# Performance work log

Measured on AMD Instinct MI355X. Metric: run time of the kernel, lower is better.

## Reference

```python
import jax, jax.numpy as jnp
import numpy as np

K = 10  # CSLS neighborhood size


def setup_inputs() -> dict:
    key = jax.random.key(0)
    k1, k2 = jax.random.split(key)
    N, D = 16384, 512
    Lvec = jax.random.normal(k1, (N, D), dtype=jnp.float32)
    Rvec = jax.random.normal(k2, (N, D), dtype=jnp.float32)
    return {"Lvec": Lvec, "Rvec": Rvec}


def reference(Lvec, Rvec):
    N = Lvec.shape[0]
    # L_sim[i, j] = <L_i, R_j>; R_sim = L_sim.T since both slices cover all rows
    sim = jnp.matmul(Lvec, Rvec.T)                      # [N_L, N_R]
    # CSLS penalties: mean of top-k similarities per row
    LR = jnp.mean(jax.lax.top_k(sim, K)[0], axis=-1)    # [N_L] per-L-entity top-k avg
    RL = jnp.mean(jax.lax.top_k(sim.T, K)[0], axis=-1)  # [N_R] per-R-entity top-k avg
    # Faithful to the torch epoch-0 broadcasting: both penalties broadcast over columns
    # csls[i, j] = 2 * R_sim[i, j] - LR[j] - RL[j]
    csls = 2.0 * sim.T - LR[None, :] - RL[None, :]      # [N_R, N_L]
    order = jnp.argsort(-csls, axis=-1)                 # descending rank lists
    # rank position of the true answer (column i for row i)
    ranks = jnp.argmax(order == jnp.arange(N)[:, None], axis=-1)  # [N] int
    top1_val = jnp.max(csls, axis=-1)                   # top-1 CSLS score per row
    return (ranks.astype(jnp.int32), top1_val)
```

## Files before the change

kernel.cpp:

```cpp
#include <hip/hip_runtime.h>
#include <hip/hip_bf16.h>
#include <hip/hip_fp8.h>
#include <stdint.h>

#define NN 16384
#define DD 512
#define BM 128
#define BN 256
#define NCT2 64
#define KT 4
#define PPW 260
#define NEG_INF (-3.0e38f)


typedef unsigned short u16;
typedef _Float16 f16;
typedef __attribute__((ext_vector_type(8))) __bf16 bf16x8;
typedef __attribute__((ext_vector_type(8))) short sh8;
typedef __attribute__((ext_vector_type(8))) _Float16 f16x8;
typedef __attribute__((ext_vector_type(4))) float f32x4;

__device__ __forceinline__ u16 f2bf(float f) {
  uint32_t x = __float_as_uint(f);
  x += 0x7fffu + ((x >> 16) & 1u);
  return (u16)(x >> 16);
}
__device__ __forceinline__ float bf2f(u16 u) {
  return __uint_as_float(((uint32_t)u) << 16);
}
__device__ __forceinline__ float f16bits(uint32_t bits) {
  f16 h;
  u16 b = (u16)bits;
  __builtin_memcpy(&h, &b, 2);
  return (float)h;
}
__device__ __forceinline__ u16 h2bits(f16 h) {
  u16 b;
  __builtin_memcpy(&b, &h, 2);
  return b;
}
__device__ __forceinline__ uint8_t f2fp8(float f) {
  __hip_fp8_e4m3 h(f);
  return (uint8_t)h.__x;
}
__device__ __forceinline__ float fp82f(uint8_t b) {
  __hip_fp8_e4m3 h;
  h.__x = (__hip_fp8_storage_t)b;
  return (float)h;
}
__device__ __forceinline__ uint32_t pk4_fp8(float a, float b, float c, float d) {
#if defined(__has_builtin) && __has_builtin(__builtin_amdgcn_cvt_pk_fp8_f32)
  int v = __builtin_amdgcn_cvt_pk_fp8_f32(a, b, 0, false);
  v = __builtin_amdgcn_cvt_pk_fp8_f32(c, d, v, true);
  return (uint32_t)v;
#else
  return (uint32_t)f2fp8(a) | ((uint32_t)f2fp8(b) << 8) |
         ((uint32_t)f2fp8(c) << 16) | ((uint32_t)f2fp8(d) << 24);
#endif
}
__device__ __forceinline__ uint32_t pkrtz(float a, float b) {
  uint32_t d;
  asm("v_cvt_pkrtz_f16_f32 %0, %1, %2" : "=v"(d) : "v"(a), "v"(b));
  return d;
}
__device__ __forceinline__ uint32_t pk_max16(uint32_t a, uint32_t b) {
  uint32_t d;
  asm("v_pk_max_f16 %0, %1, %2" : "=v"(d) : "v"(a), "v"(b));
  return d;
}
__device__ __forceinline__ uint32_t pk_min16(uint32_t a, uint32_t b) {
  uint32_t d;
  asm("v_pk_min_f16 %0, %1, %2" : "=v"(d) : "v"(a), "v"(b));
  return d;
}

__device__ __forceinline__ void gload_lds16(const u16* g, u16* lds) {
  __builtin_amdgcn_global_load_lds(
      (const __attribute__((address_space(1))) uint32_t*)g,
      (__attribute__((address_space(3))) uint32_t*)lds,
      16, 0, 0);
}

template <int N>
__device__ __forceinline__ void insN(float (&t)[N], float v) {
  #pragma unroll
  for (int j = 0; j < N; ++j) {
    float hi = fmaxf(t[j], v);
    v = fminf(t[j], v);
    t[j] = hi;
  }
}
template <int N>
__device__ __forceinline__ void pinsN(uint32_t (&t)[N], uint32_t v) {
  #pragma unroll
  for (int j = 0; j < N; ++j) {
    uint32_t hi = pk_max16(t[j], v);
    v = pk_min16(t[j], v);
    t[j] = hi;
  }
}

__global__ __launch_bounds__(256) void cast_kernel(const float* __restrict__ src,
                                                   u16* __restrict__ dst) {
  int i = (blockIdx.x * 256 + threadIdx.x) * 8;
  const float4* s4 = reinterpret_cast<const float4*>(src + i);
  float4 a = s4[0], b = s4[1];
  sh8 o;
  o[0] = (short)f2bf(a.x); o[1] = (short)f2bf(a.y);
  o[2] = (short)f2bf(a.z); o[3] = (short)f2bf(a.w);
  o[4] = (short)f2bf(b.x); o[5] = (short)f2bf(b.y);
  o[6] = (short)f2bf(b.z); o[7] = (short)f2bf(b.w);
  *reinterpret_cast<sh8*>(dst + i) = o;
}

__global__ __launch_bounds__(256) void diag_kernel(const u16* __restrict__ Lb,
                                                   const u16* __restrict__ Rb,
                                                   float* __restrict__ diag) {
  int r = blockIdx.x * 4 + (threadIdx.x >> 6);
  int lane = threadIdx.x & 63;
  sh8 a = *reinterpret_cast<const sh8*>(Lb + (size_t)r * DD + lane * 8);
  sh8 b = *reinterpret_cast<const sh8*>(Rb + (size_t)r * DD + lane * 8);
  float s = 0.f;
  #pragma unroll
  for (int j = 0; j < 8; ++j) s += bf2f((u16)a[j]) * bf2f((u16)b[j]);
  #pragma unroll
  for (int off = 32; off > 0; off >>= 1) s += __shfl_down(s, off);
  if (lane == 0) diag[r] = s;
}

#define DECODE_TILE(ct0)                                \
  const int xcd = blockIdx.x & 7;                       \
  const int idx = blockIdx.x >> 3;                      \
  const int rowtile = xcd * 16 + (idx & 15);            \
  const int coltile = (ct0) + (idx >> 4);               \
  const int rowbase = rowtile * BM;                     \
  const int colbase = coltile * BN;                     \
  const int tid = threadIdx.x;                          \
  const int w = tid >> 6;                               \
  const int lane = tid & 63;                            \
  const int quad = lane >> 4;                           \
  const int l16 = lane & 15;                            \
  const int wr = (w >> 2) * 64;                         \
  const int wc = (w & 3) * 64;                          \
  (void)xcd; (void)lane;

#define GEMM_PRE()                                                              \
  const int rp0_ = tid >> 3, gp0_ = (tid & 7) ^ (rp0_ & 7);                     \
  const int grow0_ = rp0_ * 2 + (gp0_ >> 2), gcol0_ = (gp0_ & 3) * 8;           \
  const int gl1_ = tid + 512;                                                   \
  const int rp1_ = gl1_ >> 3, gp1_ = (gl1_ & 7) ^ (rp1_ & 7);                   \
  const int grow1_ = rp1_ * 2 + (gp1_ >> 2), gcol1_ = (gp1_ & 3) * 8;           \
  const u16* gA_  = A + (size_t)(rowbase + grow0_) * DD + gcol0_;               \
  const u16* gB0_ = B + (size_t)(colbase + grow0_) * DD + gcol0_;               \
  const u16* gB1_ = B + (size_t)(colbase + grow1_) * DD + gcol1_;               \
  const int gsel_ = ((((l16) & 1) << 2) + quad) ^ (l16 >> 1);                   \
  const int rdA_ = (wr / 2 + (l16 >> 1)) * 64 + gsel_ * 8;                      \
  const int rdB_ = (wc / 2 + (l16 >> 1)) * 64 + gsel_ * 8;

#define STAGE(t, dA, dB)                                                        \
  gload_lds16(gA_  + (t) * 32, (dA) + tid * 8);                                 \
  gload_lds16(gB0_ + (t) * 32, (dB) + tid * 8);                                 \
  gload_lds16(gB1_ + (t) * 32, (dB) + 4096 + tid * 8);

#define GEMM_K_LOOP(smembase)                                                   \
  f32x4 acc[4][4];                                                              \
  _Pragma("unroll")                                                             \
  for (int a_ = 0; a_ < 4; ++a_)                                                \
    _Pragma("unroll")                                                           \
    for (int b_ = 0; b_ < 4; ++b_) acc[a_][b_] = (f32x4){0.f, 0.f, 0.f, 0.f};   \
  {                                                                             \
    GEMM_PRE()                                                                  \
    u16* const bA_[3] = {(smembase), (smembase) + 4096, (smembase) + 8192};     \
    u16* const bB_[3] = {(smembase) + 12288, (smembase) + 20480,                \
                         (smembase) + 28672};                                   \
    STAGE(0, bA_[0], bB_[0])                                                    \
    STAGE(1, bA_[1], bB_[1])                                                    \
    _Pragma("unroll")                                                           \
    for (int t = 0; t < 16; ++t) {                                              \
      if (t < 15) { asm volatile("s_waitcnt vmcnt(3)" ::: "memory"); }          \
      else        { asm volatile("s_waitcnt vmcnt(0)" ::: "memory"); }          \
      __builtin_amdgcn_s_barrier();                                             \
      asm volatile("" ::: "memory");                                            \
      {                                                                         \
        const int cs_ = t % 3;                                                  \
        const u16* cA_ = bA_[cs_];                                              \
        const u16* cB_ = bB_[cs_];                                              \
        bf16x8 af[4], bfv[4];                                                   \
        _Pragma("unroll")                                                       \
        for (int f = 0; f < 4; ++f)                                             \
          af[f]  = *reinterpret_cast<const bf16x8*>(cA_ + rdA_ + f * 512);      \
        _Pragma("unroll")                                                       \
        for (int f = 0; f < 4; ++f)                                             \
          bfv[f] = *reinterpret_cast<const bf16x8*>(cB_ + rdB_ + f * 512);      \
        __builtin_amdgcn_s_setprio(1);                                          \
        _Pragma("unroll")                                                       \
        for (int fr = 0; fr < 4; ++fr)                                          \
          _Pragma("unroll")                                                     \
          for (int fc = 0; fc < 4; ++fc)                                        \
            acc[fr][fc] = __builtin_amdgcn_mfma_f32_16x16x32_bf16(af[fr], bfv[fc], acc[fr][fc], 0, 0, 0); \
        __builtin_amdgcn_s_setprio(0);                                          \
      }                                                                         \
      asm volatile("" ::: "memory");                                            \
      if (t + 2 < 16) {                                                         \
        const int ns_ = (t + 2) % 3;                                            \
        STAGE(t + 2, bA_[ns_], bB_[ns_])                                        \
      }                                                                         \
    }                                                                           \
  }

__global__ __launch_bounds__(512, 4) void gemm_topk(const u16* __restrict__ A,
                                                    const u16* __restrict__ B,
                                                    f16* __restrict__ rowp,
                                                    f16* __restrict__ colp,
                                                    uint8_t* __restrict__ sim,
                                                    int SC2) {
  __shared__ __align__(16) u16 smem[36864];
  DECODE_TILE(0)
  GEMM_K_LOOP(smem)

  __syncthreads();
  uint32_t* hC32 = reinterpret_cast<uint32_t*>(smem);
  #pragma unroll
  for (int fr = 0; fr < 4; ++fr) {
    const int rpb = (wr + 16 * fr) / 2 + quad * 2;
    #pragma unroll
    for (int fc = 0; fc < 4; ++fc) {
      const int c = wc + 16 * fc + l16;
      hC32[rpb * PPW + c]       = pkrtz(acc[fr][fc][0], acc[fr][fc][1]);
      hC32[(rpb + 1) * PPW + c] = pkrtz(acc[fr][fc][2], acc[fr][fc][3]);
    }
  }
  __syncthreads();
  if (coltile < SC2) {
    const int SW = SC2 * BN;
    uint8_t* gs = sim + (size_t)rowbase * SW + (size_t)coltile * BN;
    const int rp0s = tid >> 6, cb = tid & 63;
    #pragma unroll
    for (int itw = 0; itw < 8; ++itw) {
      const int rp = rp0s + itw * 8;
      uint4 v = *reinterpret_cast<const uint4*>(&hC32[rp * PPW + cb * 4]);
      uint32_t d0 = v.x, d1 = v.y, d2 = v.z, d3 = v.w;
      uint32_t r0 = pk4_fp8(f16bits(d0), f16bits(d1), f16bits(d2), f16bits(d3));
      uint32_t r1 = pk4_fp8(f16bits(d0 >> 16), f16bits(d1 >> 16),
                            f16bits(d2 >> 16), f16bits(d3 >> 16));
      *reinterpret_cast<uint32_t*>(gs + (size_t)(2 * rp) * SW + cb * 4) = r0;
      *reinterpret_cast<uint32_t*>(gs + (size_t)(2 * rp + 1) * SW + cb * 4) = r1;
    }
  }
  uint32_t trow[KT];
  #pragma unroll
  for (int j = 0; j < KT; ++j) trow[j] = 0xFBFFFBFFu;
  const int rsp = tid >> 3, ce = tid & 7;
  #pragma unroll
  for (int k = 0; k < 8; ++k) {
    uint4 ch = *reinterpret_cast<const uint4*>(&hC32[rsp * PPW + ce * 32 + k * 4]);
    pinsN<KT>(trow, ch.x);
    pinsN<KT>(trow, ch.y);
    pinsN<KT>(trow, ch.z);
    pinsN<KT>(trow, ch.w);
  }
  uint32_t tcol[KT];
  #pragma unroll
  for (int j = 0; j < KT; ++j) tcol[j] = 0xFBFFFBFFu;
  const int cc = tid & 255, rph = tid >> 8;
  #pragma unroll 8
  for (int i = 0; i < 32; ++i) {
    uint32_t v = hC32[(rph * 32 + i) * PPW + cc];
    pinsN<KT>(tcol, v);
  }
  __syncthreads();
  uint32_t* sRl = hC32;
  uint32_t* sCl = hC32 + 64 * 8 * KT;
  #pragma unroll
  for (int j = 0; j < KT; ++j) sRl[(rsp * 8 + ce) * KT + j] = trow[j];
  #pragma unroll
  for (int j = 0; j < KT; ++j) sCl[(cc * 2 + rph) * KT + j] = tcol[j];
  __syncthreads();
  if (tid < 256) {
    float best[KT];
    #pragma unroll
    for (int j = 0; j < KT; ++j) best[j] = NEG_INF;
    for (int rh = 0; rh < 2; ++rh)
      for (int par = 0; par < 2; ++par)
        for (int j = 0; j < KT; ++j) {
          uint32_t u = sCl[(tid * 2 + rh) * KT + j];
          float v = f16bits(par ? (u >> 16) : u);
          if (v > best[KT - 1]) insN<KT>(best, v);
          else break;
        }
    f16* o = colp + ((size_t)rowtile * NN + colbase + tid) * KT;
    uint2 ov;
    ov.x = h2bits((f16)best[0]) | ((uint32_t)h2bits((f16)best[1]) << 16);
    ov.y = h2bits((f16)best[2]) | ((uint32_t)h2bits((f16)best[3]) << 16);
    *reinterpret_cast<uint2*>(o) = ov;
  } else if (tid < 384) {
    const int r = tid - 256;
    const int rp = r >> 1, par = r & 1;
    float best[KT];
    #pragma unroll
    for (int j = 0; j < KT; ++j) best[j] = NEG_INF;
    for (int h = 0; h < 8; ++h)
      for (int j = 0; j < KT; ++j) {
        uint32_t u = sRl[(rp * 8 + h) * KT + j];
        float v = f16bits(par ? (u >> 16) : u);
        if (v > best[KT - 1]) insN<KT>(best, v);
        else break;
      }
    f16* o = rowp + ((size_t)coltile * NN + rowbase + r) * KT;
    uint2 ov;
    ov.x = h2bits((f16)best[0]) | ((uint32_t)h2bits((f16)best[1]) << 16);
    ov.y = h2bits((f16)best[2]) | ((uint32_t)h2bits((f16)best[3]) << 16);
    *reinterpret_cast<uint2*>(o) = ov;
  }
}

__global__ __launch_bounds__(512, 4) void gemm_rank(const u16* __restrict__ A,
                                                    const u16* __restrict__ B,
                                                    const float* __restrict__ p,
                                                    const float* __restrict__ thr,
                                                    int* __restrict__ cnt_out,
                                                    float* __restrict__ mx_out,
                                                    int ct0) {
  __shared__ __align__(16) u16 smem[36864];
  DECODE_TILE(ct0)

  GEMM_K_LOOP(smem)

  float thrv[16];
  #pragma unroll
  for (int i = 0; i < 16; ++i)
    thrv[i] = thr[rowbase + wr + 16 * (i >> 2) + quad * 4 + (i & 3)];
  float pv[4];
  #pragma unroll
  for (int fc = 0; fc < 4; ++fc) pv[fc] = p[colbase + wc + 16 * fc + l16];

  int cnt[16];
  float mx[16];
  #pragma unroll
  for (int i = 0; i < 16; ++i) { cnt[i] = 0; mx[i] = NEG_INF; }
  #pragma unroll
  for (int fc = 0; fc < 4; ++fc)
    #pragma unroll
    for (int fr = 0; fr < 4; ++fr)
      #pragma unroll
      for (int reg = 0; reg < 4; ++reg) {
        float t2 = 2.f * acc[fr][fc][reg] - pv[fc];
        int idx2 = fr * 4 + reg;
        cnt[idx2] += (t2 > thrv[idx2]) ? 1 : 0;
        mx[idx2] = fmaxf(mx[idx2], t2);
      }

  __syncthreads();
  float* sMx = reinterpret_cast<float*>(smem);
  int*   sCn = reinterpret_cast<int*>(smem) + 512;
  #pragma unroll
  for (int idx2 = 0; idx2 < 16; ++idx2) {
    int c = cnt[idx2];
    float m = mx[idx2];
    #pragma unroll
    for (int off = 1; off < 16; off <<= 1) {
      c += __shfl_xor(c, off);
      m = fmaxf(m, __shfl_xor(m, off));
    }
    if (l16 == 0) {
      int rloc = 16 * (idx2 >> 2) + quad * 4 + (idx2 & 3);
      sMx[w * 64 + rloc] = m;
      sCn[w * 64 + rloc] = c;
    }
  }
  __syncthreads();
  if (tid < 128) {
    int g0 = (tid >> 6) * 4, rloc = tid & 63;
    int c = 0;
    float m = NEG_INF;
    #pragma unroll
    for (int k = 0; k < 4; ++k) {
      c += sCn[(g0 + k) * 64 + rloc];
      m = fmaxf(m, sMx[(g0 + k) * 64 + rloc]);
    }
    cnt_out[(size_t)coltile * NN + rowbase + tid] = c;
    mx_out[(size_t)coltile * NN + rowbase + tid] = m;
  }
}

__global__ __launch_bounds__(256) void scan_kernel(const uint8_t* __restrict__ sim,
                                                   const float* __restrict__ p,
                                                   const float* __restrict__ thr,
                                                   int SC2,
                                                   int* __restrict__ cnt_s,
                                                   float* __restrict__ mx_s) {
  const int tid = threadIdx.x;
  const int row0 = blockIdx.x * 4;
  const int SW = SC2 * BN;
  float t[4];
  #pragma unroll
  for (int r = 0; r < 4; ++r) t[r] = thr[row0 + r];
  int cnt[4] = {0, 0, 0, 0};
  float m[4] = {NEG_INF, NEG_INF, NEG_INF, NEG_INF};
  for (int c0 = tid * 16; c0 < SW; c0 += 4096) {
    float pv[16];
    {
      const float4* p4 = reinterpret_cast<const float4*>(p + c0);
      *reinterpret_cast<float4*>(&pv[0])  = p4[0];
      *reinterpret_cast<float4*>(&pv[4])  = p4[1];
      *reinterpret_cast<float4*>(&pv[8])  = p4[2];
      *reinterpret_cast<float4*>(&pv[12]) = p4[3];
    }
    #pragma unroll
    for (int r = 0; r < 4; ++r) {
      uint4 v = *reinterpret_cast<const uint4*>(sim + (size_t)(row0 + r) * SW + c0);
      uint32_t wds[4] = {v.x, v.y, v.z, v.w};
      #pragma unroll
      for (int j = 0; j < 16; ++j) {
        float sv = fp82f((uint8_t)(wds[j >> 2] >> ((j & 3) * 8)));
        float t2 = 2.f * sv - pv[j];
        cnt[r] += (t2 > t[r]) ? 1 : 0;
        m[r] = fmaxf(m[r], t2);
      }
    }
  }
  __shared__ float sM[4][4];
  __shared__ int sC[4][4];
  const int lane = tid & 63, w = tid >> 6;
  #pragma unroll
  for (int r = 0; r < 4; ++r) {
    int c = cnt[r];
    float mm = m[r];
    #pragma unroll
    for (int off = 32; off > 0; off >>= 1) {
      c += __shfl_down(c, off);
      mm = fmaxf(mm, __shfl_down(mm, off));
    }
    if (lane == 0) { sC[r][w] = c; sM[r][w] = mm; }
  }
  __syncthreads();
  if (tid < 4) {
    int c = sC[tid][0] + sC[tid][1] + sC[tid][2] + sC[tid][3];
    float mm = fmaxf(fmaxf(sM[tid][0], sM[tid][1]), fmaxf(sM[tid][2], sM[tid][3]));
    cnt_s[row0 + tid] = c;
    mx_s[row0 + tid] = mm;
  }
}

__global__ __launch_bounds__(256) void p_kernel(const f16* __restrict__ rowp,
                                                const f16* __restrict__ colp,
                                                const float* __restrict__ diag,
                                                float* __restrict__ pout,
                                                float* __restrict__ throut) {
  __shared__ float sB1[64][4][10];
  __shared__ float sB2[64][4][10];
  const int tid = threadIdx.x;
  const int lent = tid >> 2, part = tid & 3;
  const int l = blockIdx.x * 64 + lent;
  float b1[10], b2[10];
  #pragma unroll
  for (int j = 0; j < 10; ++j) { b1[j] = NEG_INF; b2[j] = NEG_INF; }
  for (int s = part * 16; s < part * 16 + 16; ++s) {
    uint2 u2 = *reinterpret_cast<const uint2*>(rowp + ((size_t)s * NN + l) * KT);
    uint32_t ud[2] = {u2.x, u2.y};
    #pragma unroll
    for (int d = 0; d < 2; ++d) {
      uint32_t u = ud[d];
      float v0 = f16bits(u), v1 = f16bits(u >> 16);
      if (v0 > b1[9]) insN<10>(b1, v0); else break;
      if (v1 > b1[9]) insN<10>(b1, v1); else break;
    }
  }
  for (int s = part * 32; s < part * 32 + 32; ++s) {
    uint2 u2 = *reinterpret_cast<const uint2*>(colp + ((size_t)s * NN + l) * KT);
    uint32_t ud[2] = {u2.x, u2.y};
    #pragma unroll
    for (int d = 0; d < 2; ++d) {
      uint32_t u = ud[d];
      float v0 = f16bits(u), v1 = f16bits(u >> 16);
      if (v0 > b2[9]) insN<10>(b2, v0); else break;
      if (v1 > b2[9]) insN<10>(b2, v1); else break;
    }
  }
  #pragma unroll
  for (int j = 0; j < 10; ++j) { sB1[lent][part][j] = b1[j]; sB2[lent][part][j] = b2[j]; }
  __syncthreads();
  if (tid < 64) {
    const int l2 = blockIdx.x * 64 + tid;
    float m1[10], m2[10];
    #pragma unroll
    for (int j = 0; j < 10; ++j) { m1[j] = NEG_INF; m2[j] = NEG_INF; }
    for (int pa = 0; pa < 4; ++pa) {
      for (int j = 0; j < 10; ++j) {
        float v = sB1[tid][pa][j];
        if (v > m1[9]) insN<10>(m1, v); else break;
      }
      for (int j = 0; j < 10; ++j) {
        float v = sB2[tid][pa][j];
        if (v > m2[9]) insN<10>(m2, v); else break;
      }
    }
    float s1 = 0.f, s2 = 0.f;
    #pragma unroll
    for (int j = 0; j < 10; ++j) { s1 += m1[j]; s2 += m2[j]; }
    float pv = (s1 + s2) * 0.1f;
    pout[l2] = pv;
    throut[l2] = 2.f * diag[l2] - pv;
  }
}

__global__ __launch_bounds__(256) void final_kernel(const int* __restrict__ cnt,
                                                    const float* __restrict__ mx,
                                                    const int* __restrict__ cnt_s,
                                                    const float* __restrict__ mx_s,
                                                    int sc2,
                                                    float* __restrict__ out) {
  int r = blockIdx.x * 256 + threadIdx.x;
  int c = 0;
  float m = NEG_INF;
  if (sc2 > 0) { c = cnt_s[r]; m = mx_s[r]; }
  for (int s = sc2; s < NCT2; ++s) {
    c += cnt[(size_t)s * NN + r];
    m = fmaxf(m, mx[(size_t)s * NN + r]);
  }
  out[r] = (float)c;
  out[NN + r] = m;
}

extern "C" void kernel_launch(void* const* d_in, const int* in_sizes, int n_in,
                              void* d_out, int out_size, void* d_ws, size_t ws_size,
                              hipStream_t stream) {
  const float* L = (const float*)d_in[0];
  const float* R = (const float*)d_in[1];
  char* ws = (char*)d_ws;

  const size_t PART_ROW = (size_t)NCT2 * NN * KT * 2;
  const size_t PART_COL = (size_t)128 * NN * KT * 2;
  const size_t TAILOFF = (32ull << 20) + PART_ROW + PART_COL;
  const size_t SIMOFF = TAILOFF + (320ull << 10);

  u16* Lb   = (u16*)ws;
  u16* Rb   = (u16*)(ws + (16ull << 20));
  f16* rowp = (f16*)(ws + (32ull << 20));
  f16* colp = (f16*)(ws + (32ull << 20) + PART_ROW);
  char* tail = ws + TAILOFF;
  float* diag   = (float*)tail;
  float* pbuf   = (float*)(tail + (64ull << 10));
  float* thrbuf = (float*)(tail + (128ull << 10));
  int*   cnt_s  = (int*)(tail + (192ull << 10));
  float* mx_s   = (float*)(tail + (256ull << 10));
  uint8_t* sim  = (uint8_t*)(ws + SIMOFF);
  int*   cntp = (int*)rowp;
  float* mxp  = (float*)colp;

  int SC2 = 0;
  if (ws_size > SIMOFF) {
    size_t sc = (ws_size - SIMOFF) / ((size_t)NN * BN * 1);
    if (sc > 64) sc = 64;
    SC2 = (int)sc;
  }

  cast_kernel<<<(NN * DD / (256 * 8)), 256, 0, stream>>>(L, Lb);
  cast_kernel<<<(NN * DD / (256 * 8)), 256, 0, stream>>>(R, Rb);
  diag_kernel<<<NN / 4, 256, 0, stream>>>(Lb, Rb, diag);
  gemm_topk<<<(NN / BM) * NCT2, 512, 0, stream>>>(Rb, Lb, rowp, colp, sim, SC2);
  p_kernel<<<NN / 64, 256, 0, stream>>>(rowp, colp, diag, pbuf, thrbuf);
  if (SC2 > 0)
    scan_kernel<<<NN / 4, 256, 0, stream>>>(sim, pbuf, thrbuf, SC2, cnt_s, mx_s);
  if (SC2 < NCT2)
    gemm_rank<<<(NN / BM) * (NCT2 - SC2), 512, 0, stream>>>(Rb, Lb, pbuf, thrbuf,
                                                            cntp, mxp, SC2);
  final_kernel<<<NN / 256, 256, 0, stream>>>(cntp, mxp, cnt_s, mx_s, SC2,
                                             (float*)d_out);
}
```

Baseline: 569.3 us.

## Fuse preprocessing kernels, merge scan and rank GEMM, reorder prefetch

```diff
diff --git a/kernel.cpp b/kernel.cpp
--- a/kernel.cpp
+++ b/kernel.cpp
@@ -100,32 +100,39 @@
   }
 }
 
-__global__ __launch_bounds__(256) void cast_kernel(const float* __restrict__ src,
-                                                   u16* __restrict__ dst) {
-  int i = (blockIdx.x * 256 + threadIdx.x) * 8;
-  const float4* s4 = reinterpret_cast<const float4*>(src + i);
-  float4 a = s4[0], b = s4[1];
-  sh8 o;
-  o[0] = (short)f2bf(a.x); o[1] = (short)f2bf(a.y);
-  o[2] = (short)f2bf(a.z); o[3] = (short)f2bf(a.w);
-  o[4] = (short)f2bf(b.x); o[5] = (short)f2bf(b.y);
-  o[6] = (short)f2bf(b.z); o[7] = (short)f2bf(b.w);
-  *reinterpret_cast<sh8*>(dst + i) = o;
-}
-
-__global__ __launch_bounds__(256) void diag_kernel(const u16* __restrict__ Lb,
-                                                   const u16* __restrict__ Rb,
-                                                   float* __restrict__ diag) {
-  int r = blockIdx.x * 4 + (threadIdx.x >> 6);
-  int lane = threadIdx.x & 63;
-  sh8 a = *reinterpret_cast<const sh8*>(Lb + (size_t)r * DD + lane * 8);
-  sh8 b = *reinterpret_cast<const sh8*>(Rb + (size_t)r * DD + lane * 8);
-  float s = 0.f;
-  #pragma unroll
-  for (int j = 0; j < 8; ++j) s += bf2f((u16)a[j]) * bf2f((u16)b[j]);
-  #pragma unroll
-  for (int off = 32; off > 0; off >>= 1) s += __shfl_down(s, off);
-  if (lane == 0) diag[r] = s;
+__global__ __launch_bounds__(256) void fused_pre(const float* __restrict__ L,
+                                                 const float* __restrict__ R,
+                                                 u16* __restrict__ Lb,
+                                                 u16* __restrict__ Rb,
+                                                 float* __restrict__ diag) {
+  const int b = blockIdx.x;
+  const int tid = threadIdx.x;
+  if (b < 8192) {
+    const float* src = (b < 4096) ? L : R;
+    u16* dst = (b < 4096) ? Lb : Rb;
+    int bb = (b < 4096) ? b : b - 4096;
+    int i = (bb * 256 + tid) * 8;
+    const float4* s4 = reinterpret_cast<const float4*>(src + i);
+    float4 a = s4[0], c = s4[1];
+    sh8 o;
+    o[0] = (short)f2bf(a.x); o[1] = (short)f2bf(a.y);
+    o[2] = (short)f2bf(a.z); o[3] = (short)f2bf(a.w);
+    o[4] = (short)f2bf(c.x); o[5] = (short)f2bf(c.y);
+    o[6] = (short)f2bf(c.z); o[7] = (short)f2bf(c.w);
+    *reinterpret_cast<sh8*>(dst + i) = o;
+  } else {
+    int db = b - 8192;
+    int r = db * 4 + (tid >> 6);
+    int lane = tid & 63;
+    const float4* la = reinterpret_cast<const float4*>(L + (size_t)r * DD + lane * 8);
+    const float4* rb = reinterpret_cast<const float4*>(R + (size_t)r * DD + lane * 8);
+    float4 a0 = la[0], a1 = la[1], b0 = rb[0], b1 = rb[1];
+    float s = a0.x * b0.x + a0.y * b0.y + a0.z * b0.z + a0.w * b0.w +
+              a1.x * b1.x + a1.y * b1.y + a1.z * b1.z + a1.w * b1.w;
+    #pragma unroll
+    for (int off = 32; off > 0; off >>= 1) s += __shfl_down(s, off);
+    if (lane == 0) diag[r] = s;
+  }
 }
 
 #define DECODE_TILE(ct0)                                \
@@ -192,6 +199,10 @@
         _Pragma("unroll")                                                       \
         for (int f = 0; f < 4; ++f)                                             \
           bfv[f] = *reinterpret_cast<const bf16x8*>(cB_ + rdB_ + f * 512);      \
+        if (t + 2 < 16) {                                                       \
+          const int ns_ = (t + 2) % 3;                                          \
+          STAGE(t + 2, bA_[ns_], bB_[ns_])                                      \
+        }                                                                       \
         __builtin_amdgcn_s_setprio(1);                                          \
         _Pragma("unroll")                                                       \
         for (int fr = 0; fr < 4; ++fr)                                          \
@@ -201,10 +212,6 @@
         __builtin_amdgcn_s_setprio(0);                                          \
       }                                                                         \
       asm volatile("" ::: "memory");                                            \
-      if (t + 2 < 16) {                                                         \
-        const int ns_ = (t + 2) % 3;                                            \
-        STAGE(t + 2, bA_[ns_], bB_[ns_])                                        \
-      }                                                                         \
     }                                                                           \
   }
 
@@ -314,131 +321,136 @@
   }
 }
 
-__global__ __launch_bounds__(512, 4) void gemm_rank(const u16* __restrict__ A,
-                                                    const u16* __restrict__ B,
-                                                    const float* __restrict__ p,
-                                                    const float* __restrict__ thr,
-                                                    int* __restrict__ cnt_out,
-                                                    float* __restrict__ mx_out,
-                                                    int ct0) {
+__global__ __launch_bounds__(512, 4) void fused_post(const u16* __restrict__ A,
+                                                     const u16* __restrict__ B,
+                                                     const float* __restrict__ p,
+                                                     const float* __restrict__ thr,
+                                                     const uint8_t* __restrict__ sim,
+                                                     int SC2, int NR,
+                                                     int* __restrict__ cnt_out,
+                                                     float* __restrict__ mx_out,
+                                                     int* __restrict__ cnt_s,
+                                                     float* __restrict__ mx_s) {
   __shared__ __align__(16) u16 smem[36864];
-  DECODE_TILE(ct0)
-
-  GEMM_K_LOOP(smem)
-
-  float thrv[16];
-  #pragma unroll
-  for (int i = 0; i < 16; ++i)
-    thrv[i] = thr[rowbase + wr + 16 * (i >> 2) + quad * 4 + (i & 3)];
-  float pv[4];
-  #pragma unroll
-  for (int fc = 0; fc < 4; ++fc) pv[fc] = p[colbase + wc + 16 * fc + l16];
-
-  int cnt[16];
-  float mx[16];
-  #pragma unroll
-  for (int i = 0; i < 16; ++i) { cnt[i] = 0; mx[i] = NEG_INF; }
-  #pragma unroll
-  for (int fc = 0; fc < 4; ++fc)
-    #pragma unroll
-    for (int fr = 0; fr < 4; ++fr)
+  if ((int)blockIdx.x < NR * 128) {
+    DECODE_TILE(SC2)
+    GEMM_K_LOOP(smem)
+
+    float thrv[16];
+    #pragma unroll
+    for (int i = 0; i < 16; ++i)
+      thrv[i] = thr[rowbase + wr + 16 * (i >> 2) + quad * 4 + (i & 3)];
+    float pv[4];
+    #pragma unroll
+    for (int fc = 0; fc < 4; ++fc) pv[fc] = p[colbase + wc + 16 * fc + l16];
+
+    int cnt[16];
+    float mx[16];
+    #pragma unroll
+    for (int i = 0; i < 16; ++i) { cnt[i] = 0; mx[i] = NEG_INF; }
+    #pragma unroll
+    for (int fc = 0; fc < 4; ++fc)
       #pragma unroll
-      for (int reg = 0; reg < 4; ++reg) {
-        float t2 = 2.f * acc[fr][fc][reg] - pv[fc];
-        int idx2 = fr * 4 + reg;
-        cnt[idx2] += (t2 > thrv[idx2]) ? 1 : 0;
-        mx[idx2] = fmaxf(mx[idx2], t2);
-      }
-
-  __syncthreads();
-  float* sMx = reinterpret_cast<float*>(smem);
-  int*   sCn = reinterpret_cast<int*>(smem) + 512;
-  #pragma unroll
-  for (int idx2 = 0; idx2 < 16; ++idx2) {
-    int c = cnt[idx2];
-    float m = mx[idx2];
-    #pragma unroll
-    for (int off = 1; off < 16; off <<= 1) {
-      c += __shfl_xor(c, off);
-      m = fmaxf(m, __shfl_xor(m, off));
-    }
-    if (l16 == 0) {
-      int rloc = 16 * (idx2 >> 2) + quad * 4 + (idx2 & 3);
-      sMx[w * 64 + rloc] = m;
-      sCn[w * 64 + rloc] = c;
-    }
-  }
-  __syncthreads();
-  if (tid < 128) {
-    int g0 = (tid >> 6) * 4, rloc = tid & 63;
-    int c = 0;
-    float m = NEG_INF;
-    #pragma unroll
-    for (int k = 0; k < 4; ++k) {
-      c += sCn[(g0 + k) * 64 + rloc];
-      m = fmaxf(m, sMx[(g0 + k) * 64 + rloc]);
-    }
-    cnt_out[(size_t)coltile * NN + rowbase + tid] = c;
-    mx_out[(size_t)coltile * NN + rowbase + tid] = m;
-  }
-}
-
-__global__ __launch_bounds__(256) void scan_kernel(const uint8_t* __restrict__ sim,
-                                                   const float* __restrict__ p,
-                                                   const float* __restrict__ thr,
-                                                   int SC2,
-                                                   int* __restrict__ cnt_s,
-                                                   float* __restrict__ mx_s) {
-  const int tid = threadIdx.x;
-  const int row0 = blockIdx.x * 4;
-  const int SW = SC2 * BN;
-  float t[4];
-  #pragma unroll
-  for (int r = 0; r < 4; ++r) t[r] = thr[row0 + r];
-  int cnt[4] = {0, 0, 0, 0};
-  float m[4] = {NEG_INF, NEG_INF, NEG_INF, NEG_INF};
-  for (int c0 = tid * 16; c0 < SW; c0 += 4096) {
-    float pv[16];
-    {
-      const float4* p4 = reinterpret_cast<const float4*>(p + c0);
-      *reinterpret_cast<float4*>(&pv[0])  = p4[0];
-      *reinterpret_cast<float4*>(&pv[4])  = p4[1];
-      *reinterpret_cast<float4*>(&pv[8])  = p4[2];
-      *reinterpret_cast<float4*>(&pv[12]) = p4[3];
-    }
-    #pragma unroll
-    for (int r = 0; r < 4; ++r) {
-      uint4 v = *reinterpret_cast<const uint4*>(sim + (size_t)(row0 + r) * SW + c0);
-      uint32_t wds[4] = {v.x, v.y, v.z, v.w};
+      for (int fr = 0; fr < 4; ++fr)
+        #pragma unroll
+        for (int reg = 0; reg < 4; ++reg) {
+          float t2 = 2.f * acc[fr][fc][reg] - pv[fc];
+          int idx2 = fr * 4 + reg;
+          cnt[idx2] += (t2 > thrv[idx2]) ? 1 : 0;
+          mx[idx2] = fmaxf(mx[idx2], t2);
+        }
+
+    __syncthreads();
+    float* sMx = reinterpret_cast<float*>(smem);
+    int*   sCn = reinterpret_cast<int*>(smem) + 512;
+    #pragma unroll
+    for (int idx2 = 0; idx2 < 16; ++idx2) {
+      int c = cnt[idx2];
+      float m = mx[idx2];
       #pragma unroll
-      for (int j = 0; j < 16; ++j) {
-        float sv = fp82f((uint8_t)(wds[j >> 2] >> ((j & 3) * 8)));
-        float t2 = 2.f * sv - pv[j];
-        cnt[r] += (t2 > t[r]) ? 1 : 0;
-        m[r] = fmaxf(m[r], t2);
-      }
-    }
-  }
-  __shared__ float sM[4][4];
-  __shared__ int sC[4][4];
-  const int lane = tid & 63, w = tid >> 6;
-  #pragma unroll
-  for (int r = 0; r < 4; ++r) {
-    int c = cnt[r];
-    float mm = m[r];
-    #pragma unroll
-    for (int off = 32; off > 0; off >>= 1) {
-      c += __shfl_down(c, off);
-      mm = fmaxf(mm, __shfl_down(mm, off));
-    }
-    if (lane == 0) { sC[r][w] = c; sM[r][w] = mm; }
-  }
-  __syncthreads();
-  if (tid < 4) {
-    int c = sC[tid][0] + sC[tid][1] + sC[tid][2] + sC[tid][3];
-    float mm = fmaxf(fmaxf(sM[tid][0], sM[tid][1]), fmaxf(sM[tid][2], sM[tid][3]));
-    cnt_s[row0 + tid] = c;
-    mx_s[row0 + tid] = mm;
+      for (int off = 1; off < 16; off <<= 1) {
+        c += __shfl_xor(c, off);
+        m = fmaxf(m, __shfl_xor(m, off));
+      }
+      if (l16 == 0) {
+        int rloc = 16 * (idx2 >> 2) + quad * 4 + (idx2 & 3);
+        sMx[w * 64 + rloc] = m;
+        sCn[w * 64 + rloc] = c;
+      }
+    }
+    __syncthreads();
+    if (tid < 128) {
+      int g0 = (tid >> 6) * 4, rloc = tid & 63;
+      int c = 0;
+      float m = NEG_INF;
+      #pragma unroll
+      for (int k = 0; k < 4; ++k) {
+        c += sCn[(g0 + k) * 64 + rloc];
+        m = fmaxf(m, sMx[(g0 + k) * 64 + rloc]);
+      }
+      cnt_out[(size_t)coltile * NN + rowbase + tid] = c;
+      mx_out[(size_t)coltile * NN + rowbase + tid] = m;
+    }
+  } else {
+    const int tid = threadIdx.x;
+    const int sblk = blockIdx.x - NR * 128;
+    const int row0 = sblk * 8;
+    const int SW = SC2 * BN;
+    float t[8];
+    #pragma unroll
+    for (int r = 0; r < 8; ++r) t[r] = thr[row0 + r];
+    int cnt[8];
+    float m[8];
+    #pragma unroll
+    for (int r = 0; r < 8; ++r) { cnt[r] = 0; m[r] = NEG_INF; }
+    for (int c0 = tid * 16; c0 < SW; c0 += 8192) {
+      float pv[16];
+      {
+        const float4* p4 = reinterpret_cast<const float4*>(p + c0);
+        *reinterpret_cast<float4*>(&pv[0])  = p4[0];
+        *reinterpret_cast<float4*>(&pv[4])  = p4[1];
+        *reinterpret_cast<float4*>(&pv[8])  = p4[2];
+        *reinterpret_cast<float4*>(&pv[12]) = p4[3];
+      }
+      #pragma unroll
+      for (int r = 0; r < 8; ++r) {
+        uint4 v = *reinterpret_cast<const uint4*>(sim + (size_t)(row0 + r) * SW + c0);
+        uint32_t wds[4] = {v.x, v.y, v.z, v.w};
+        #pragma unroll
+        for (int j = 0; j < 16; ++j) {
+          float sv = fp82f((uint8_t)(wds[j >> 2] >> ((j & 3) * 8)));
+          float t2 = 2.f * sv - pv[j];
+          cnt[r] += (t2 > t[r]) ? 1 : 0;
+          m[r] = fmaxf(m[r], t2);
+        }
+      }
+    }
+    float* sM = reinterpret_cast<float*>(smem);
+    int*   sC = reinterpret_cast<int*>(smem) + 64;
+    const int lane = tid & 63, wv = tid >> 6;
+    #pragma unroll
+    for (int r = 0; r < 8; ++r) {
+      int c = cnt[r];
+      float mm = m[r];
+      #pragma unroll
+      for (int off = 32; off > 0; off >>= 1) {
+        c += __shfl_down(c, off);
+        mm = fmaxf(mm, __shfl_down(mm, off));
+      }
+      if (lane == 0) { sC[r * 8 + wv] = c; sM[r * 8 + wv] = mm; }
+    }
+    __syncthreads();
+    if (tid < 8) {
+      int c = 0;
+      float mm = NEG_INF;
+      #pragma unroll
+      for (int k = 0; k < 8; ++k) {
+        c += sC[tid * 8 + k];
+        mm = fmaxf(mm, sM[tid * 8 + k]);
+      }
+      cnt_s[row0 + tid] = c;
+      mx_s[row0 + tid] = mm;
+    }
   }
 }
 
@@ -447,15 +459,15 @@
                                                 const float* __restrict__ diag,
                                                 float* __restrict__ pout,
                                                 float* __restrict__ throut) {
-  __shared__ float sB1[64][4][10];
-  __shared__ float sB2[64][4][10];
+  __shared__ float sB1[32][8][10];
+  __shared__ float sB2[32][8][10];
   const int tid = threadIdx.x;
-  const int lent = tid >> 2, part = tid & 3;
-  const int l = blockIdx.x * 64 + lent;
+  const int lent = tid >> 3, part = tid & 7;
+  const int l = blockIdx.x * 32 + lent;
   float b1[10], b2[10];
   #pragma unroll
   for (int j = 0; j < 10; ++j) { b1[j] = NEG_INF; b2[j] = NEG_INF; }
-  for (int s = part * 16; s < part * 16 + 16; ++s) {
+  for (int s = part * 8; s < part * 8 + 8; ++s) {
     uint2 u2 = *reinterpret_cast<const uint2*>(rowp + ((size_t)s * NN + l) * KT);
     uint32_t ud[2] = {u2.x, u2.y};
     #pragma unroll
@@ -466,7 +478,7 @@
       if (v1 > b1[9]) insN<10>(b1, v1); else break;
     }
   }
-  for (int s = part * 32; s < part * 32 + 32; ++s) {
+  for (int s = part * 16; s < part * 16 + 16; ++s) {
     uint2 u2 = *reinterpret_cast<const uint2*>(colp + ((size_t)s * NN + l) * KT);
     uint32_t ud[2] = {u2.x, u2.y};
     #pragma unroll
@@ -480,12 +492,12 @@
   #pragma unroll
   for (int j = 0; j < 10; ++j) { sB1[lent][part][j] = b1[j]; sB2[lent][part][j] = b2[j]; }
   __syncthreads();
-  if (tid < 64) {
-    const int l2 = blockIdx.x * 64 + tid;
+  if (tid < 32) {
+    const int l2 = blockIdx.x * 32 + tid;
     float m1[10], m2[10];
     #pragma unroll
     for (int j = 0; j < 10; ++j) { m1[j] = NEG_INF; m2[j] = NEG_INF; }
-    for (int pa = 0; pa < 4; ++pa) {
+    for (int pa = 0; pa < 8; ++pa) {
       for (int j = 0; j < 10; ++j) {
         float v = sB1[tid][pa][j];
         if (v > m1[9]) insN<10>(m1, v); else break;
@@ -554,17 +566,17 @@
     if (sc > 64) sc = 64;
     SC2 = (int)sc;
   }
-
-  cast_kernel<<<(NN * DD / (256 * 8)), 256, 0, stream>>>(L, Lb);
-  cast_kernel<<<(NN * DD / (256 * 8)), 256, 0, stream>>>(R, Rb);
-  diag_kernel<<<NN / 4, 256, 0, stream>>>(Lb, Rb, diag);
+  const int NR = NCT2 - SC2;
+
+  fused_pre<<<12288, 256, 0, stream>>>(L, R, Lb, Rb, diag);
   gemm_topk<<<(NN / BM) * NCT2, 512, 0, stream>>>(Rb, Lb, rowp, colp, sim, SC2);
-  p_kernel<<<NN / 64, 256, 0, stream>>>(rowp, colp, diag, pbuf, thrbuf);
-  if (SC2 > 0)
-    scan_kernel<<<NN / 4, 256, 0, stream>>>(sim, pbuf, thrbuf, SC2, cnt_s, mx_s);
-  if (SC2 < NCT2)
-    gemm_rank<<<(NN / BM) * (NCT2 - SC2), 512, 0, stream>>>(Rb, Lb, pbuf, thrbuf,
-                                                            cntp, mxp, SC2);
+  p_kernel<<<NN / 32, 256, 0, stream>>>(rowp, colp, diag, pbuf, thrbuf);
+  {
+    int grid = NR * 128 + (SC2 > 0 ? (NN / 8) : 0);
+    if (grid > 0)
+      fused_post<<<grid, 512, 0, stream>>>(Rb, Lb, pbuf, thrbuf, sim, SC2, NR,
+                                           cntp, mxp, cnt_s, mx_s);
+  }
   final_kernel<<<NN / 256, 256, 0, stream>>>(cntp, mxp, cnt_s, mx_s, SC2,
                                              (float*)d_out);
 }
```

Result: slower. 688.5 us (+20.9%).
